# Kernel optimization log

Hardware: AMD Instinct MI355X
Metric: run time of the kernel (lower is better)

The kernel has to match this reference:

```python
import jax, jax.numpy as jnp
import numpy as np

EPS = 1e-6
NH, D_NOPE, D_ROPE, DV = 16, 128, 64, 128
DQK = D_NOPE + D_ROPE  # 192
KV_LORA = 512
Q_LORA = 1536
TOP_K, N_GROUP, TOPK_GROUP, N_EXP = 2, 4, 2, 8
INTER = 768
SCALING = DQK ** -0.5  # rope_scaling is None -> no yarn mscale
RSF = 2.5  # routed_scaling_factor


def rms_norm(x, w):
    v = jnp.mean(jnp.square(x), axis=-1, keepdims=True)
    return x * jax.lax.rsqrt(v + EPS) * w


def rotate_half(x):
    x1, x2 = jnp.split(x, 2, axis=-1)
    return jnp.concatenate([-x2, x1], axis=-1)


def interleave(x):
    # view(b,h,s,d//2,2).transpose(4,3).reshape(b,h,s,d): evens then odds
    b, h, s, d = x.shape
    return x.reshape(b, h, s, d // 2, 2).swapaxes(-1, -2).reshape(b, h, s, d)


def mlp(x, gw, uw, dw):
    return (jax.nn.silu(x @ gw.T) * (x @ uw.T)) @ dw.T


def setup_inputs() -> dict:
    key = jax.random.key(0)
    ks = jax.random.split(key, 16)
    B, S, H = 2, 1024, 2048
    sd = 0.02

    def p(k, shape):
        return jax.random.normal(k, shape, jnp.float32) * sd

    # standard RoPE cos/sin table
    inv_freq = 1.0 / (10000.0 ** (jnp.arange(0, D_ROPE, 2, dtype=jnp.float32) / D_ROPE))
    pos = jnp.arange(S, dtype=jnp.float32)
    freqs = pos[:, None] * inv_freq[None, :]
    emb = jnp.concatenate([freqs, freqs], axis=-1)  # [S, D_ROPE]
    cos = jnp.broadcast_to(jnp.cos(emb)[None], (B, S, D_ROPE))
    sin = jnp.broadcast_to(jnp.sin(emb)[None], (B, S, D_ROPE))

    return dict(
        hidden_states=jax.random.normal(ks[0], (B, S, H), jnp.float32),
        cos=cos,
        sin=sin,
        ln1_w=jnp.ones((H,), jnp.float32),
        q_a_w=p(ks[1], (Q_LORA, H)),
        q_a_ln_w=jnp.ones((Q_LORA,), jnp.float32),
        q_b_w=p(ks[2], (NH * DQK, Q_LORA)),
        kv_a_w=p(ks[3], (KV_LORA + D_ROPE, H)),
        kv_a_ln_w=jnp.ones((KV_LORA,), jnp.float32),
        kv_b_w=p(ks[4], (NH * (D_NOPE + DV), KV_LORA)),
        o_w=p(ks[5], (H, NH * DV)),
        ln2_w=jnp.ones((H,), jnp.float32),
        router_w=p(ks[6], (N_EXP, H)),
        router_bias=jnp.zeros((N_EXP,), jnp.float32),
        gate_w=p(ks[7], (N_EXP, INTER, H)),
        up_w=p(ks[8], (N_EXP, INTER, H)),
        down_w=p(ks[9], (N_EXP, H, INTER)),
        sh_gate_w=p(ks[10], (INTER, H)),
        sh_up_w=p(ks[11], (INTER, H)),
        sh_down_w=p(ks[12], (H, INTER)),
    )


def reference(hidden_states, cos, sin, ln1_w, q_a_w, q_a_ln_w, q_b_w, kv_a_w,
              kv_a_ln_w, kv_b_w, o_w, ln2_w, router_w, router_bias,
              gate_w, up_w, down_w, sh_gate_w, sh_up_w, sh_down_w):
    B, S, H = hidden_states.shape
    # ----- input_layernorm + MLA attention -----
    resid = hidden_states
    x = rms_norm(hidden_states, ln1_w)

    q = rms_norm(x @ q_a_w.T, q_a_ln_w) @ q_b_w.T       # [B,S,NH*DQK]
    q = q.reshape(B, S, NH, DQK).transpose(0, 2, 1, 3)   # [B,NH,S,DQK]
    q_pass, q_rot = q[..., :D_NOPE], q[..., D_NOPE:]

    ckv = x @ kv_a_w.T                                   # [B,S,KV_LORA+D_ROPE]
    k_pass_c, k_rot = ckv[..., :KV_LORA], ckv[..., KV_LORA:]
    kv = rms_norm(k_pass_c, kv_a_ln_w) @ kv_b_w.T        # [B,S,NH*(D_NOPE+DV)]
    kv = kv.reshape(B, S, NH, D_NOPE + DV).transpose(0, 2, 1, 3)
    k_pass, v = kv[..., :D_NOPE], kv[..., D_NOPE:]

    k_rot = k_rot.reshape(B, 1, S, D_ROPE)
    c = cos[:, None]  # [B,1,S,D_ROPE]
    s_ = sin[:, None]
    q_rot = interleave(q_rot)
    k_rot = interleave(k_rot)
    q_rot = q_rot * c + rotate_half(q_rot) * s_
    k_rot = k_rot * c + rotate_half(k_rot) * s_
    k_rot = jnp.broadcast_to(k_rot, (B, NH, S, D_ROPE))

    qs = jnp.concatenate([q_pass, q_rot], axis=-1)       # [B,NH,S,DQK]
    ks = jnp.concatenate([k_pass, k_rot], axis=-1)

    scores = jnp.einsum('bhqd,bhkd->bhqk', qs, ks) * SCALING
    causal = jnp.tril(jnp.ones((S, S), dtype=bool))
    scores = jnp.where(causal, scores, -jnp.inf)
    probs = jax.nn.softmax(scores, axis=-1)
    attn = jnp.einsum('bhqk,bhkd->bhqd', probs, v)
    attn = attn.transpose(0, 2, 1, 3).reshape(B, S, NH * DV)
    x = resid + attn @ o_w.T

    # ----- post_attention_layernorm + MoE -----
    resid = x
    h = rms_norm(x, ln2_w)
    t = h.reshape(-1, H)

    # router (fp32)
    scores_r = jax.nn.sigmoid(t.astype(jnp.float32) @ router_w.T.astype(jnp.float32))
    sc = scores_r + router_bias[None, :]
    gs = sc.reshape(-1, N_GROUP, N_EXP // N_GROUP)
    group_scores = jax.lax.top_k(gs, 2)[0].sum(-1)          # [T,G]
    gidx = jax.lax.top_k(group_scores, TOPK_GROUP)[1]
    gmask = jax.nn.one_hot(gidx, N_GROUP).sum(1)            # [T,G]
    emask = jnp.repeat(gmask, N_EXP // N_GROUP, axis=-1)    # [T,E]
    masked = jnp.where(emask > 0, sc, 0.0)
    idx = jax.lax.top_k(masked, TOP_K)[1]                   # [T,k]
    w = jnp.take_along_axis(scores_r, idx, axis=-1)
    w = w / (w.sum(-1, keepdims=True) + 1e-20) * RSF

    # routed experts: dense-all-experts compute, then routed-weight combine
    gate_h = jnp.einsum('td,eid->tei', t, gate_w)
    up_h = jnp.einsum('td,eid->tei', t, up_w)
    eo = jnp.einsum('tei,edi->ted', jax.nn.silu(gate_h) * up_h, down_w)
    dense_w = (jax.nn.one_hot(idx, N_EXP) * w[..., None]).sum(1)  # [T,E]
    moe_out = jnp.einsum('ted,te->td', eo, dense_w).reshape(B, S, H)

    shared = mlp(h, sh_gate_w, sh_up_w, sh_down_w)
    return resid + moe_out + shared
```

## Files before the change

### kernel.cpp

```cpp
#include <hip/hip_runtime.h>

typedef float f4 __attribute__((ext_vector_type(4)));
typedef float f32x4 __attribute__((ext_vector_type(4)));
typedef unsigned short us8 __attribute__((ext_vector_type(8)));
typedef __bf16 bf8 __attribute__((ext_vector_type(8)));

static constexpr int B_ = 2, S_ = 1024, H_ = 2048, T_ = B_ * S_;
static constexpr int NH_ = 16, DN_ = 128, DR_ = 64, DV_ = 128, DQK_ = 192;
static constexpr int KVL_ = 512, QL_ = 1536, INTER_ = 768, NEXP_ = 8, NE9_ = 9;
static constexpr int QKA_ = 2176;
static constexpr float SCALING_ = 0.07216878364870322f;
static constexpr float EPS_ = 1e-6f;

__device__ __forceinline__ unsigned short f2bf(float f) {
    unsigned u = __float_as_uint(f);
    u += 0x7fffu + ((u >> 16) & 1u);
    return (unsigned short)(u >> 16);
}
__device__ __forceinline__ float bf2f(unsigned short h) {
    return __uint_as_float(((unsigned)h) << 16);
}
__device__ __forceinline__ us8 pack8(f4 a, f4 b) {
    us8 r;
    r[0] = f2bf(a[0]); r[1] = f2bf(a[1]); r[2] = f2bf(a[2]); r[3] = f2bf(a[3]);
    r[4] = f2bf(b[0]); r[5] = f2bf(b[1]); r[6] = f2bf(b[2]); r[7] = f2bf(b[3]);
    return r;
}

__device__ __forceinline__ void gload16(const unsigned short* g, unsigned short* lds) {
    __builtin_amdgcn_global_load_lds(
        (const __attribute__((address_space(1))) void*)g,
        (__attribute__((address_space(3))) void*)lds, 16, 0, 0);
}

template <int MODE>
__global__ __launch_bounds__(256) void gemm2(
    const unsigned short* __restrict__ A, const unsigned short* __restrict__ Bw,
    float* __restrict__ Cf, unsigned short* __restrict__ Cb,
    const float* __restrict__ add,
    const int* __restrict__ cnt, const int* __restrict__ off,
    int M, int N, int K, int ldA, long sB)
{
    constexpr int BM = 128, BN = 128, BK = 64;
    __shared__ __align__(16) unsigned short As[2][BM * BK];
    __shared__ __align__(16) unsigned short Bs[2][BN * BK];
    const int tid = threadIdx.x, lane = tid & 63, wv = tid >> 6;
    const int wm = (wv >> 1) * 64, wn = (wv & 1) * 64;

    const int nb = gridDim.x * gridDim.y;
    const int lin = blockIdx.y * gridDim.x + blockIdx.x;
    const int swz = (lin & 7) * (nb >> 3) + (lin >> 3);
    const int bx = swz % gridDim.x;
    const int by = swz / gridDim.x;
    const int m0 = bx * BM, n0 = by * BN;

    int mcnt = M, obase = 0;
    if constexpr (MODE == 2) {
        mcnt = cnt[blockIdx.z];
        if (m0 >= mcnt) return;
        obase = off[blockIdx.z];
    }

    const int srow = tid >> 3;
    const int scol = (((tid & 7) ^ (srow & 7)) * 8);
    long aoff[4], boff[4];
#pragma unroll
    for (int s = 0; s < 4; s++) {
        int r = m0 + s * 32 + srow;
        if constexpr (MODE == 2) {
            aoff[s] = (long)(obase + r) * ldA + scol;
        } else {
            aoff[s] = (long)r * ldA + scol;
        }
        boff[s] = (long)blockIdx.z * sB + (long)(n0 + s * 32 + srow) * K + scol;
    }

    f32x4 acc[4][4];
#pragma unroll
    for (int m = 0; m < 4; m++)
#pragma unroll
        for (int n = 0; n < 4; n++) acc[m][n] = f32x4{0.f, 0.f, 0.f, 0.f};

    const int fr = lane & 15, lg = lane >> 4;
    const int xr = fr & 7;

    auto stage = [&](int buf, int k0) {
#pragma unroll
        for (int s = 0; s < 4; s++)
            gload16(A + aoff[s] + k0, &As[buf][s * 2048 + wv * 512]);
#pragma unroll
        for (int s = 0; s < 4; s++)
            gload16(Bw + boff[s] + k0, &Bs[buf][s * 2048 + wv * 512]);
    };
    auto compute = [&](int buf) {
        __builtin_amdgcn_s_setprio(1);
        bf8 af[4][2], bfv[4][2];
#pragma unroll
        for (int m = 0; m < 4; m++) {
            int R = wm + m * 16 + fr;
#pragma unroll
            for (int ks = 0; ks < 2; ks++)
                af[m][ks] = *(const bf8*)&As[buf][R * 64 + ((ks * 4 + lg) ^ xr) * 8];
        }
#pragma unroll
        for (int n = 0; n < 4; n++) {
            int R = wn + n * 16 + fr;
#pragma unroll
            for (int ks = 0; ks < 2; ks++)
                bfv[n][ks] = *(const bf8*)&Bs[buf][R * 64 + ((ks * 4 + lg) ^ xr) * 8];
        }
#pragma unroll
        for (int m = 0; m < 4; m++)
#pragma unroll
            for (int n = 0; n < 4; n++) {
                acc[m][n] = __builtin_amdgcn_mfma_f32_16x16x32_bf16(af[m][0], bfv[n][0], acc[m][n], 0, 0, 0);
                acc[m][n] = __builtin_amdgcn_mfma_f32_16x16x32_bf16(af[m][1], bfv[n][1], acc[m][n], 0, 0, 0);
            }
        __builtin_amdgcn_s_setprio(0);
    };

    const int nt = K / BK;
    stage(0, 0);
    for (int t = 0; t < nt; t++) {
        if (t + 1 < nt) {
            stage((t & 1) ^ 1, (t + 1) * BK);
            asm volatile("s_waitcnt vmcnt(8)" ::: "memory");
        } else {
            asm volatile("s_waitcnt vmcnt(0)" ::: "memory");
        }
        __builtin_amdgcn_s_barrier();
        compute(t & 1);
        __builtin_amdgcn_s_barrier();
    }

#pragma unroll
    for (int m = 0; m < 4; m++) {
#pragma unroll
        for (int n = 0; n < 4; n++) {
#pragma unroll
            for (int i = 0; i < 4; i++) {
                int row = wm + m * 16 + lg * 4 + i;
                int col = n0 + wn + n * 16 + fr;
                float v = acc[m][n][i];
                if constexpr (MODE == 0) {
                    long idx = (long)(m0 + row) * N + col;
                    if (Cb)       Cb[idx] = f2bf(v);
                    else if (add) Cf[idx] = v + add[idx];
                    else          Cf[idx] = v;
                } else {
                    if (m0 + row < mcnt)
                        Cb[(long)(obase + m0 + row) * N + col] = f2bf(v);
                }
            }
        }
    }
}

__global__ __launch_bounds__(256) void gemm_gu(
    const unsigned short* __restrict__ A, const unsigned short* __restrict__ Bw,
    unsigned short* __restrict__ actm,
    const int* __restrict__ cnt, const int* __restrict__ off,
    const int* __restrict__ idxl)
{
    constexpr int BM = 64, BN = 64, BK = 64, K = H_;
    __shared__ __align__(16) unsigned short As[2][BM * BK];
    __shared__ __align__(16) unsigned short Bg[2][BN * BK];
    __shared__ __align__(16) unsigned short Bu[2][BN * BK];
    const int tid = threadIdx.x, lane = tid & 63, wv = tid >> 6;
    const int wm = (wv >> 1) * 32, wn = (wv & 1) * 32;

    const int nb = gridDim.x * gridDim.y;
    const int lin = blockIdx.y * gridDim.x + blockIdx.x;
    const int swz = (lin & 7) * (nb >> 3) + (lin >> 3);
    const int bx = swz % gridDim.x;
    const int by = swz / gridDim.x;
    const int m0 = bx * BM, n0 = by * BN;
    const int e = blockIdx.z;

    const int mcnt = cnt[e];
    if (m0 >= mcnt) return;
    const int obase = off[e];

    const int srow = tid >> 3;
    const int scol = (((tid & 7) ^ (srow & 7)) * 8);
    long aoff[2], bgo[2], buo[2];
#pragma unroll
    for (int s = 0; s < 2; s++) {
        int r = m0 + s * 32 + srow;
        int rc = (r < mcnt) ? r : mcnt - 1;
        aoff[s] = (long)idxl[(long)e * T_ + rc] * H_ + scol;
        bgo[s] = ((long)e * (2 * INTER_) + n0 + s * 32 + srow) * K + scol;
        buo[s] = ((long)e * (2 * INTER_) + INTER_ + n0 + s * 32 + srow) * K + scol;
    }

    f32x4 ag[2][2], au[2][2];
#pragma unroll
    for (int m = 0; m < 2; m++)
#pragma unroll
        for (int n = 0; n < 2; n++) {
            ag[m][n] = f32x4{0.f, 0.f, 0.f, 0.f};
            au[m][n] = f32x4{0.f, 0.f, 0.f, 0.f};
        }

    const int fr = lane & 15, lg = lane >> 4;
    const int xr = fr & 7;

    auto stage = [&](int buf, int k0) {
#pragma unroll
        for (int s = 0; s < 2; s++)
            gload16(A + aoff[s] + k0, &As[buf][s * 2048 + wv * 512]);
#pragma unroll
        for (int s = 0; s < 2; s++)
            gload16(Bw + bgo[s] + k0, &Bg[buf][s * 2048 + wv * 512]);
#pragma unroll
        for (int s = 0; s < 2; s++)
            gload16(Bw + buo[s] + k0, &Bu[buf][s * 2048 + wv * 512]);
    };
    auto compute = [&](int buf) {
        __builtin_amdgcn_s_setprio(1);
        bf8 af[2][2], bgf[2][2], buf_[2][2];
#pragma unroll
        for (int m = 0; m < 2; m++) {
            int R = wm + m * 16 + fr;
#pragma unroll
            for (int ks = 0; ks < 2; ks++)
                af[m][ks] = *(const bf8*)&As[buf][R * 64 + ((ks * 4 + lg) ^ xr) * 8];
        }
#pragma unroll
        for (int n = 0; n < 2; n++) {
            int R = wn + n * 16 + fr;
#pragma unroll
            for (int ks = 0; ks < 2; ks++) {
                bgf[n][ks] = *(const bf8*)&Bg[buf][R * 64 + ((ks * 4 + lg) ^ xr) * 8];
                buf_[n][ks] = *(const bf8*)&Bu[buf][R * 64 + ((ks * 4 + lg) ^ xr) * 8];
            }
        }
#pragma unroll
        for (int m = 0; m < 2; m++)
#pragma unroll
            for (int n = 0; n < 2; n++) {
                ag[m][n] = __builtin_amdgcn_mfma_f32_16x16x32_bf16(af[m][0], bgf[n][0], ag[m][n], 0, 0, 0);
                ag[m][n] = __builtin_amdgcn_mfma_f32_16x16x32_bf16(af[m][1], bgf[n][1], ag[m][n], 0, 0, 0);
                au[m][n] = __builtin_amdgcn_mfma_f32_16x16x32_bf16(af[m][0], buf_[n][0], au[m][n], 0, 0, 0);
                au[m][n] = __builtin_amdgcn_mfma_f32_16x16x32_bf16(af[m][1], buf_[n][1], au[m][n], 0, 0, 0);
            }
        __builtin_amdgcn_s_setprio(0);
    };

    const int nt = K / BK;
    stage(0, 0);
    for (int t = 0; t < nt; t++) {
        if (t + 1 < nt) {
            stage((t & 1) ^ 1, (t + 1) * BK);
            asm volatile("s_waitcnt vmcnt(6)" ::: "memory");
        } else {
            asm volatile("s_waitcnt vmcnt(0)" ::: "memory");
        }
        __builtin_amdgcn_s_barrier();
        compute(t & 1);
        __builtin_amdgcn_s_barrier();
    }

#pragma unroll
    for (int m = 0; m < 2; m++) {
#pragma unroll
        for (int n = 0; n < 2; n++) {
#pragma unroll
            for (int i = 0; i < 4; i++) {
                int row = wm + m * 16 + lg * 4 + i;
                if (m0 + row < mcnt) {
                    float g = ag[m][n][i], u = au[m][n][i];
                    float v = g / (1.f + __expf(-g)) * u;
                    actm[(long)(obase + m0 + row) * INTER_ + n0 + wn + n * 16 + fr] = f2bf(v);
                }
            }
        }
    }
}

__global__ __launch_bounds__(256) void fa_k(
    const unsigned short* __restrict__ qs, const unsigned short* __restrict__ ks,
    const unsigned short* __restrict__ vt, unsigned short* __restrict__ ab)
{
    constexpr int KB = 64;
    const int q0 = blockIdx.x * 64;
    const int bh = blockIdx.y;
    const int b = bh >> 4, h = bh & 15;
    const int tid = threadIdx.x, lane = tid & 63, wv = tid >> 6;
    const int fr = lane & 15, lg = lane >> 4;
    const int ko = lg * 8;

    __shared__ __align__(16) unsigned short Kl[KB][200];
    __shared__ __align__(16) unsigned short Vl[128][72];
    __shared__ __align__(16) unsigned short Pl[4][16][72];

    const unsigned short* qp = qs + ((long)bh * S_ + q0 + wv * 16 + fr) * DQK_ + ko;
    bf8 qf[6];
#pragma unroll
    for (int s = 0; s < 6; s++) qf[s] = *(const bf8*)(qp + s * 32);

    f32x4 o[8];
#pragma unroll
    for (int n = 0; n < 8; n++) o[n] = f32x4{0.f, 0.f, 0.f, 0.f};
    float mrow[4] = {-3e38f, -3e38f, -3e38f, -3e38f};
    float lrow[4] = {0.f, 0.f, 0.f, 0.f};

    const int nt = q0 / KB + 1;

    const unsigned short* kg = ks + ((long)bh * S_ + (tid >> 2)) * DQK_ + (tid & 3) * 48;
    const unsigned short* vg = vt + ((long)bh * DV_ + (tid >> 1)) * S_ + (tid & 1) * 32;

    us8 krg[6], vrg[4];
#pragma unroll
    for (int j = 0; j < 6; j++) krg[j] = *(const us8*)(kg + j * 8);
#pragma unroll
    for (int j = 0; j < 4; j++) vrg[j] = *(const us8*)(vg + j * 8);

    for (int t = 0; t < nt; t++) {
        __syncthreads();
        {
            int r = tid >> 2, c = (tid & 3) * 48;
#pragma unroll
            for (int j = 0; j < 6; j++) *(us8*)&Kl[r][c + j * 8] = krg[j];
            int dv = tid >> 1, c2 = (tid & 1) * 32;
#pragma unroll
            for (int j = 0; j < 4; j++) *(us8*)&Vl[dv][c2 + j * 8] = vrg[j];
        }
        __syncthreads();
        if (t + 1 < nt) {
            long kof = (long)(t + 1) * KB;
#pragma unroll
            for (int j = 0; j < 6; j++) krg[j] = *(const us8*)(kg + kof * DQK_ + j * 8);
#pragma unroll
            for (int j = 0; j < 4; j++) vrg[j] = *(const us8*)(vg + kof + j * 8);
        }
        f32x4 ps[4];
#pragma unroll
        for (int ct = 0; ct < 4; ct++) {
            f32x4 a = f32x4{0.f, 0.f, 0.f, 0.f};
#pragma unroll
            for (int s = 0; s < 6; s++) {
                bf8 kf = *(const bf8*)&Kl[ct * 16 + fr][s * 32 + ko];
                a = __builtin_amdgcn_mfma_f32_16x16x32_bf16(qf[s], kf, a, 0, 0, 0);
            }
            ps[ct] = a;
        }
        const int kv0 = t * KB;
        const bool diag = (kv0 == q0);
#pragma unroll
        for (int ct = 0; ct < 4; ct++)
#pragma unroll
            for (int i = 0; i < 4; i++) {
                float v = ps[ct][i] * SCALING_;
                if (diag && (kv0 + ct * 16 + fr) > (q0 + wv * 16 + lg * 4 + i)) v = -3e38f;
                ps[ct][i] = v;
            }
        float scl[4];
#pragma unroll
        for (int i = 0; i < 4; i++) {
            float v = fmaxf(fmaxf(ps[0][i], ps[1][i]), fmaxf(ps[2][i], ps[3][i]));
#pragma unroll
            for (int x = 8; x; x >>= 1) v = fmaxf(v, __shfl_xor(v, x, 16));
            float mn = fmaxf(mrow[i], v);
            scl[i] = __expf(mrow[i] - mn);
            mrow[i] = mn;
        }
        float tsum[4] = {0.f, 0.f, 0.f, 0.f};
#pragma unroll
        for (int ct = 0; ct < 4; ct++)
#pragma unroll
            for (int i = 0; i < 4; i++) {
                float e = __expf(ps[ct][i] - mrow[i]);
                tsum[i] += e;
                Pl[wv][lg * 4 + i][ct * 16 + fr] = f2bf(e);
            }
#pragma unroll
        for (int i = 0; i < 4; i++) {
            float v = tsum[i];
#pragma unroll
            for (int x = 8; x; x >>= 1) v += __shfl_xor(v, x, 16);
            lrow[i] = lrow[i] * scl[i] + v;
        }
#pragma unroll
        for (int n = 0; n < 8; n++)
#pragma unroll
            for (int i = 0; i < 4; i++) o[n][i] *= scl[i];
        bf8 pf[2];
#pragma unroll
        for (int ksl = 0; ksl < 2; ksl++)
            pf[ksl] = *(const bf8*)&Pl[wv][fr][ksl * 32 + ko];
#pragma unroll
        for (int n = 0; n < 8; n++)
#pragma unroll
            for (int ksl = 0; ksl < 2; ksl++) {
                bf8 vf = *(const bf8*)&Vl[n * 16 + fr][ksl * 32 + ko];
                o[n] = __builtin_amdgcn_mfma_f32_16x16x32_bf16(pf[ksl], vf, o[n], 0, 0, 0);
            }
    }
#pragma unroll
    for (int i = 0; i < 4; i++) {
        float inv = 1.f / lrow[i];
        long rbase = ((long)b * S_ + q0 + wv * 16 + lg * 4 + i) * H_ + h * DV_;
#pragma unroll
        for (int n = 0; n < 8; n++)
            ab[rbase + n * 16 + fr] = f2bf(o[n][i] * inv);
    }
}

__global__ __launch_bounds__(256) void cvt_k(
    const float* __restrict__ s, unsigned short* __restrict__ d, long n)
{
    long i = ((long)blockIdx.x * 256 + threadIdx.x) * 8;
    if (i < n) {
        f4 a = *(const f4*)(s + i);
        f4 b = *(const f4*)(s + i + 4);
        *(us8*)(d + i) = pack8(a, b);
    }
}

__global__ __launch_bounds__(256) void cvt_qka_k(
    const float* __restrict__ qa, const float* __restrict__ kva,
    unsigned short* __restrict__ d)
{
    long i = ((long)blockIdx.x * 256 + threadIdx.x) * 8;
    long row = i >> 11, col = i & 2047;
    us8 o;
    if (row < QL_) {
        const float* s = qa + row * H_ + col;
        o = pack8(*(const f4*)s, *(const f4*)(s + 4));
    } else if (row < QL_ + 576) {
        const float* s = kva + (row - QL_) * H_ + col;
        o = pack8(*(const f4*)s, *(const f4*)(s + 4));
    } else {
        o = us8{0, 0, 0, 0, 0, 0, 0, 0};
    }
    *(us8*)(d + i) = o;
}

__global__ __launch_bounds__(256) void cvt_cat9_k(
    const float* __restrict__ g, const float* __restrict__ u,
    const float* __restrict__ sg, const float* __restrict__ su,
    unsigned short* __restrict__ d)
{
    long ii = ((long)blockIdx.x * 256 + threadIdx.x) * 8;
    int e = blockIdx.y;
    long row = ii >> 11, col = ii & 2047;
    const float* src;
    if (row < INTER_)
        src = (e < 8) ? (g + ((long)e * INTER_ + row) * H_ + col) : (sg + row * H_ + col);
    else
        src = (e < 8) ? (u + ((long)e * INTER_ + row - INTER_) * H_ + col)
                      : (su + (row - INTER_) * H_ + col);
    *(us8*)(d + (long)e * (2 * INTER_) * H_ + ii) = pack8(*(const f4*)src, *(const f4*)(src + 4));
}

__global__ __launch_bounds__(256) void rmsnorm_f2b(
    const float* __restrict__ in, const float* __restrict__ w,
    unsigned short* __restrict__ ob, float* __restrict__ of)
{
    const long base = (long)blockIdx.x * H_;
    const int c = threadIdx.x * 8;
    f4 v0 = *(const f4*)(in + base + c);
    f4 v1 = *(const f4*)(in + base + c + 4);
    float ss = v0[0] * v0[0] + v0[1] * v0[1] + v0[2] * v0[2] + v0[3] * v0[3]
             + v1[0] * v1[0] + v1[1] * v1[1] + v1[2] * v1[2] + v1[3] * v1[3];
#pragma unroll
    for (int o = 32; o; o >>= 1) ss += __shfl_down(ss, o);
    __shared__ float red[4];
    if ((threadIdx.x & 63) == 0) red[threadIdx.x >> 6] = ss;
    __syncthreads();
    float r = rsqrtf((red[0] + red[1] + red[2] + red[3]) / H_ + EPS_);
    f4 w0 = *(const f4*)(w + c);
    f4 w1 = *(const f4*)(w + c + 4);
    f4 a, b;
#pragma unroll
    for (int j = 0; j < 4; j++) { a[j] = v0[j] * r * w0[j]; b[j] = v1[j] * r * w1[j]; }
    *(us8*)(ob + base + c) = pack8(a, b);
    if (of) {
        *(f4*)(of + base + c) = a;
        *(f4*)(of + base + c + 4) = b;
    }
}

__global__ __launch_bounds__(256) void rmsnorm_b2b(
    const unsigned short* __restrict__ in, const float* __restrict__ w,
    unsigned short* __restrict__ out, int cols, int istride, int ostride)
{
    const long ib = (long)blockIdx.x * istride;
    const long ob = (long)blockIdx.x * ostride;
    const int nu = cols >> 3;
    float ss = 0.f;
    for (int u = threadIdx.x; u < nu; u += 256) {
        us8 v = *(const us8*)(in + ib + u * 8);
#pragma unroll
        for (int j = 0; j < 8; j++) { float f = bf2f(v[j]); ss += f * f; }
    }
#pragma unroll
    for (int o = 32; o; o >>= 1) ss += __shfl_down(ss, o);
    __shared__ float red[4];
    if ((threadIdx.x & 63) == 0) red[threadIdx.x >> 6] = ss;
    __syncthreads();
    float r = rsqrtf((red[0] + red[1] + red[2] + red[3]) / cols + EPS_);
    for (int u = threadIdx.x; u < nu; u += 256) {
        us8 v = *(const us8*)(in + ib + u * 8);
        f4 w0 = *(const f4*)(w + u * 8);
        f4 w1 = *(const f4*)(w + u * 8 + 4);
        us8 o;
#pragma unroll
        for (int j = 0; j < 4; j++) o[j] = f2bf(bf2f(v[j]) * r * w0[j]);
#pragma unroll
        for (int j = 0; j < 4; j++) o[4 + j] = f2bf(bf2f(v[4 + j]) * r * w1[j]);
        *(us8*)(out + ob + u * 8) = o;
    }
}

__global__ __launch_bounds__(64) void rope_q_k(
    const unsigned short* __restrict__ q, const float* __restrict__ cs,
    const float* __restrict__ sn, unsigned short* __restrict__ qs)
{
    int t = blockIdx.x;
    int h = t & 15;
    int bs = t >> 4;
    int s = bs & (S_ - 1);
    int b = bs >> 10;
    const unsigned short* qrow = q + (long)bs * (NH_ * DQK_) + h * DQK_;
    unsigned short* orow = qs + ((long)(b * NH_ + h) * S_ + s) * DQK_;
    int l = threadIdx.x;
    orow[l] = qrow[l];
    orow[l + 64] = qrow[l + 64];
    int j = l & 31;
    float x0 = bf2f(qrow[DN_ + 2 * j]), x1 = bf2f(qrow[DN_ + 2 * j + 1]);
    float c = cs[(long)bs * DR_ + j], si = sn[(long)bs * DR_ + j];
    if (l < 32) orow[DN_ + j] = f2bf(x0 * c - x1 * si);
    else        orow[DN_ + 32 + j] = f2bf(x1 * c + x0 * si);
}

__global__ __launch_bounds__(64) void rope_k_k(
    const unsigned short* __restrict__ qkab, const float* __restrict__ cs,
    const float* __restrict__ sn, unsigned short* __restrict__ ks)
{
    int bs = blockIdx.x;
    int s = bs & (S_ - 1);
    int b = bs >> 10;
    const unsigned short* kr = qkab + (long)bs * QKA_ + QL_ + KVL_;
    int l = threadIdx.x;
    int j = l & 31;
    float x0 = bf2f(kr[2 * j]), x1 = bf2f(kr[2 * j + 1]);
    float c = cs[(long)bs * DR_ + j], si = sn[(long)bs * DR_ + j];
    float val = (l < 32) ? (x0 * c - x1 * si) : (x1 * c + x0 * si);
    int off = (l < 32) ? (DN_ + j) : (DN_ + 32 + j);
    unsigned short bv = f2bf(val);
    for (int h = 0; h < NH_; h++)
        ks[((long)(b * NH_ + h) * S_ + s) * DQK_ + off] = bv;
}

__global__ __launch_bounds__(128) void kpass_k(
    const unsigned short* __restrict__ kv, unsigned short* __restrict__ ks)
{
    int t = blockIdx.x;
    int h = t & 15;
    int bs = t >> 4;
    int s = bs & (S_ - 1);
    int b = bs >> 10;
    ks[((long)(b * NH_ + h) * S_ + s) * DQK_ + threadIdx.x] = kv[(long)t * 256 + threadIdx.x];
}

__global__ __launch_bounds__(256) void vt_k(
    const unsigned short* __restrict__ kv, unsigned short* __restrict__ vt)
{
    __shared__ unsigned short tile[64][DV_ + 8];
    int s0 = blockIdx.x * 64;
    int bh = blockIdx.y;
    int b = bh >> 4, h = bh & 15;
#pragma unroll
    for (int it = 0; it < 4; it++) {
        int idx = it * 256 + threadIdx.x;
        int sl = idx >> 4, du = idx & 15;
        *(us8*)&tile[sl][du * 8] =
            *(const us8*)(kv + ((long)(b * S_ + s0 + sl) * NH_ + h) * 256 + DN_ + du * 8);
    }
    __syncthreads();
#pragma unroll
    for (int it = 0; it < 4; it++) {
        int idx = it * 256 + threadIdx.x;
        int d = idx >> 3, su = idx & 7;
        us8 o;
#pragma unroll
        for (int j = 0; j < 8; j++) o[j] = tile[su * 8 + j][d];
        *(us8*)(vt + ((long)bh * DV_ + d) * S_ + s0 + su * 8) = o;
    }
}

__global__ void zero9_k(int* __restrict__ cnt)
{
    if (threadIdx.x < NE9_) cnt[threadIdx.x] = (threadIdx.x == 8) ? T_ : 0;
}

__global__ void offs_k(const int* __restrict__ cnt, int* __restrict__ off)
{
    if (threadIdx.x == 0) {
        int a = 0;
        for (int e = 0; e < NE9_; e++) { off[e] = a; a += cnt[e]; }
    }
}

__global__ __launch_bounds__(64) void router_k(
    const float* __restrict__ h, const float* __restrict__ rw,
    const float* __restrict__ rb, int* __restrict__ cnt,
    int* __restrict__ idxl, int* __restrict__ tep, float* __restrict__ tww)
{
    int t = blockIdx.x;
    int l = threadIdx.x;
    const float* hr = h + (long)t * H_;
    float pe[8] = {0, 0, 0, 0, 0, 0, 0, 0};
    for (int k = l; k < H_; k += 64) {
        float hv = hr[k];
#pragma unroll
        for (int e = 0; e < 8; e++) pe[e] += hv * rw[e * H_ + k];
    }
#pragma unroll
    for (int e = 0; e < 8; e++)
        for (int o = 32; o; o >>= 1) pe[e] += __shfl_down(pe[e], o);
    if (l == 0) {
        float sr[8], sc[8];
#pragma unroll
        for (int e = 0; e < 8; e++) {
            sr[e] = 1.f / (1.f + __expf(-pe[e]));
            sc[e] = sr[e] + rb[e];
        }
        float gs[4];
        for (int g = 0; g < 4; g++) gs[g] = sc[2 * g] + sc[2 * g + 1];
        int g0 = 0;
        for (int g = 1; g < 4; g++) if (gs[g] > gs[g0]) g0 = g;
        int g1 = -1;
        for (int g = 0; g < 4; g++) {
            if (g == g0) continue;
            if (g1 < 0 || gs[g] > gs[g1]) g1 = g;
        }
        int i0 = -1, i1 = -1;
        for (int e = 0; e < 8; e++) {
            int g = e >> 1;
            if (g != g0 && g != g1) continue;
            if (i0 < 0 || sc[e] > sc[i0]) i0 = e;
        }
        for (int e = 0; e < 8; e++) {
            int g = e >> 1;
            if (g != g0 && g != g1) continue;
            if (e == i0) continue;
            if (i1 < 0 || sc[e] > sc[i1]) i1 = e;
        }
        float w0 = sr[i0], w1 = sr[i1];
        float inv = 2.5f / (w0 + w1 + 1e-20f);
        int p0 = atomicAdd(&cnt[i0], 1);
        idxl[i0 * T_ + p0] = t;
        int p1 = atomicAdd(&cnt[i1], 1);
        idxl[i1 * T_ + p1] = t;
        tep[t * 4 + 0] = i0; tep[t * 4 + 1] = p0;
        tep[t * 4 + 2] = i1; tep[t * 4 + 3] = p1;
        tww[t * 2 + 0] = w0 * inv;
        tww[t * 2 + 1] = w1 * inv;
        idxl[8 * T_ + t] = t;
    }
}

__global__ __launch_bounds__(256) void gather_k(
    const unsigned short* __restrict__ pd, const int* __restrict__ off,
    const int* __restrict__ tep, const float* __restrict__ tww,
    float* __restrict__ out)
{
    int t = blockIdx.x;
    int e0 = tep[t * 4], p0 = tep[t * 4 + 1];
    int e1 = tep[t * 4 + 2], p1 = tep[t * 4 + 3];
    float w0 = tww[t * 2], w1 = tww[t * 2 + 1];
    long r0 = (long)(off[e0] + p0) * H_;
    long r1 = (long)(off[e1] + p1) * H_;
    long rs = (long)(off[8] + t) * H_;
    int c = threadIdx.x * 8;
    us8 a = *(const us8*)(pd + r0 + c);
    us8 b = *(const us8*)(pd + r1 + c);
    us8 s = *(const us8*)(pd + rs + c);
    float* op = out + (long)t * H_ + c;
#pragma unroll
    for (int j = 0; j < 8; j++)
        op[j] += bf2f(s[j]) + w0 * bf2f(a[j]) + w1 * bf2f(b[j]);
}

extern "C" void kernel_launch(void* const* d_in, const int* in_sizes, int n_in,
                              void* d_out, int out_size, void* d_ws, size_t ws_size,
                              hipStream_t stream)
{
    const float* hidden = (const float*)d_in[0];
    const float* cosb   = (const float*)d_in[1];
    const float* sinb   = (const float*)d_in[2];
    const float* ln1w   = (const float*)d_in[3];
    const float* qaw    = (const float*)d_in[4];
    const float* qalnw  = (const float*)d_in[5];
    const float* qbw    = (const float*)d_in[6];
    const float* kvaw   = (const float*)d_in[7];
    const float* kvalnw = (const float*)d_in[8];
    const float* kvbw   = (const float*)d_in[9];
    const float* ow     = (const float*)d_in[10];
    const float* ln2w   = (const float*)d_in[11];
    const float* rw     = (const float*)d_in[12];
    const float* rb     = (const float*)d_in[13];
    const float* gw     = (const float*)d_in[14];
    const float* uw     = (const float*)d_in[15];
    const float* dwn    = (const float*)d_in[16];
    const float* sgw    = (const float*)d_in[17];
    const float* suw    = (const float*)d_in[18];
    const float* sdw    = (const float*)d_in[19];
    float* out = (float*)d_out;
    (void)in_sizes; (void)n_in; (void)out_size; (void)ws_size;

    char* ws = (char*)d_ws;
    const size_t MB = 1u << 20;
    unsigned short* qkawb = (unsigned short*)(ws + 0 * MB);
    unsigned short* qbwb  = (unsigned short*)(ws + 9 * MB);
    unsigned short* kvbwb = (unsigned short*)(ws + 18 * MB);
    unsigned short* owb   = (unsigned short*)(ws + 22 * MB);
    unsigned short* xb    = (unsigned short*)(ws + 30 * MB);
    unsigned short* qkab  = (unsigned short*)(ws + 38 * MB);
    unsigned short* qb16  = (unsigned short*)(ws + 47 * MB);
    unsigned short* ckvnb = (unsigned short*)(ws + 59 * MB);
    unsigned short* kvb   = (unsigned short*)(ws + 61 * MB);
    unsigned short* qs    = (unsigned short*)(ws + 77 * MB);
    unsigned short* ks    = (unsigned short*)(ws + 89 * MB);
    unsigned short* vt    = (unsigned short*)(ws + 30 * MB);
    unsigned short* ab    = (unsigned short*)(ws + 38 * MB);
    float* hbuf = (float*)(ws + 0 * MB);
    unsigned short* actm = (unsigned short*)(ws + 0 * MB);
    unsigned short* hb16 = (unsigned short*)(ws + 16 * MB);
    int*   cnt  = (int*)(ws + 24 * MB);
    int*   offb = (int*)(ws + 24 * MB + 256);
    int*   idxl = (int*)(ws + 24 * MB + 512);
    int*   tep  = (int*)(ws + 24 * MB + 512 + 9 * T_ * 4);
    float* tww  = (float*)(ws + 24 * MB + 512 + 9 * T_ * 4 + 4 * T_ * 4);
    unsigned short* guwb = (unsigned short*)(ws + 25 * MB);
    unsigned short* dwnb = (unsigned short*)(ws + 25 * MB);
    unsigned short* pd   = (unsigned short*)(ws + 79 * MB);

    cvt_qka_k<<<(QKA_ * H_) / 2048, 256, 0, stream>>>(qaw, kvaw, qkawb);
    cvt_k<<<(NH_ * DQK_ * QL_) / 2048, 256, 0, stream>>>(qbw, qbwb, (long)NH_ * DQK_ * QL_);
    cvt_k<<<(NH_ * 256 * KVL_) / 2048, 256, 0, stream>>>(kvbw, kvbwb, (long)NH_ * 256 * KVL_);
    cvt_k<<<(H_ * H_) / 2048, 256, 0, stream>>>(ow, owb, (long)H_ * H_);

    rmsnorm_f2b<<<T_, 256, 0, stream>>>(hidden, ln1w, xb, nullptr);

    gemm2<0><<<dim3(T_ / 128, QKA_ / 128, 1), 256, 0, stream>>>(
        xb, qkawb, nullptr, qkab, nullptr, nullptr, nullptr,
        T_, QKA_, H_, H_, 0);
    rmsnorm_b2b<<<T_, 256, 0, stream>>>(qkab, qalnw, qkab, QL_, QKA_, QKA_);
    gemm2<0><<<dim3(T_ / 128, (NH_ * DQK_) / 128, 1), 256, 0, stream>>>(
        qkab, qbwb, nullptr, qb16, nullptr, nullptr, nullptr,
        T_, NH_ * DQK_, QL_, QKA_, 0);
    rmsnorm_b2b<<<T_, 256, 0, stream>>>(qkab + QL_, kvalnw, ckvnb, KVL_, QKA_, KVL_);
    gemm2<0><<<dim3(T_ / 128, (NH_ * 256) / 128, 1), 256, 0, stream>>>(
        ckvnb, kvbwb, nullptr, kvb, nullptr, nullptr, nullptr,
        T_, NH_ * 256, KVL_, KVL_, 0);

    rope_q_k<<<T_ * NH_, 64, 0, stream>>>(qb16, cosb, sinb, qs);
    rope_k_k<<<T_, 64, 0, stream>>>(qkab, cosb, sinb, ks);
    kpass_k<<<T_ * NH_, 128, 0, stream>>>(kvb, ks);
    vt_k<<<dim3(S_ / 64, B_ * NH_), 256, 0, stream>>>(kvb, vt);

    fa_k<<<dim3(S_ / 64, B_ * NH_), 256, 0, stream>>>(qs, ks, vt, ab);

    gemm2<0><<<dim3(T_ / 128, H_ / 128, 1), 256, 0, stream>>>(
        ab, owb, out, nullptr, hidden, nullptr, nullptr,
        T_, H_, H_, H_, 0);

    rmsnorm_f2b<<<T_, 256, 0, stream>>>(out, ln2w, hb16, hbuf);
    zero9_k<<<1, 64, 0, stream>>>(cnt);
    router_k<<<T_, 64, 0, stream>>>(hbuf, rw, rb, cnt, idxl, tep, tww);
    offs_k<<<1, 64, 0, stream>>>(cnt, offb);

    cvt_cat9_k<<<dim3((2 * INTER_ * H_) / 2048, NE9_), 256, 0, stream>>>(gw, uw, sgw, suw, guwb);
    gemm_gu<<<dim3(T_ / 64, INTER_ / 64, NE9_), 256, 0, stream>>>(
        hb16, guwb, actm, cnt, offb, idxl);

    cvt_k<<<(NEXP_ * H_ * INTER_) / 2048, 256, 0, stream>>>(dwn, dwnb, (long)NEXP_ * H_ * INTER_);
    cvt_k<<<(H_ * INTER_) / 2048, 256, 0, stream>>>(sdw, dwnb + (long)NEXP_ * H_ * INTER_, (long)H_ * INTER_);

    gemm2<2><<<dim3(T_ / 128, H_ / 128, NE9_), 256, 0, stream>>>(
        actm, dwnb, nullptr, pd, nullptr, cnt, offb,
        T_, H_, INTER_, INTER_, (long)H_ * INTER_);
    gather_k<<<T_, 256, 0, stream>>>(pd, offb, tep, tww, out);
}
```

Measured before the change: 501.0 us.

## Fuse fp32 weight conversion into GEMM B-tile loads and reverse FA block order

Drops the separate fp32-to-bf16 weight conversion kernels for q_b, kv_b, o_proj, the expert gate/up and the down weights. The GEMMs now load fp32 weights into registers, pack them to bf16 and write them to LDS inside the double-buffered loop. This removes a full read-write pass over the weights and several launches. The cost is twice the B-tile global traffic per reuse, more registers, and a direct LDS write path instead of global_load_lds. The attention grid also reverses the query-block order for half the heads, presumably to balance causal workload across CUs.

```diff
diff --git a/kernel.cpp b/kernel.cpp
--- a/kernel.cpp
+++ b/kernel.cpp
@@ -33,9 +33,10 @@
         (__attribute__((address_space(3))) void*)lds, 16, 0, 0);
 }
 
-template <int MODE>
+template <int MODE, int BF32>
 __global__ __launch_bounds__(256) void gemm2(
-    const unsigned short* __restrict__ A, const unsigned short* __restrict__ Bw,
+    const unsigned short* __restrict__ A, const void* __restrict__ Bv,
+    const void* __restrict__ Bv2,
     float* __restrict__ Cf, unsigned short* __restrict__ Cb,
     const float* __restrict__ add,
     const int* __restrict__ cnt, const int* __restrict__ off,
@@ -61,6 +62,16 @@
         obase = off[blockIdx.z];
     }
 
+    const unsigned short* Bb = (const unsigned short*)Bv;
+    const float* Bf = nullptr;
+    if constexpr (BF32) {
+        if constexpr (MODE == 2)
+            Bf = (blockIdx.z < 8) ? ((const float*)Bv + (long)blockIdx.z * sB)
+                                  : (const float*)Bv2;
+        else
+            Bf = (const float*)Bv;
+    }
+
     const int srow = tid >> 3;
     const int scol = (((tid & 7) ^ (srow & 7)) * 8);
     long aoff[4], boff[4];
@@ -72,7 +83,10 @@
         } else {
             aoff[s] = (long)r * ldA + scol;
         }
-        boff[s] = (long)blockIdx.z * sB + (long)(n0 + s * 32 + srow) * K + scol;
+        if constexpr (BF32)
+            boff[s] = (long)(n0 + s * 32 + srow) * K + scol;
+        else
+            boff[s] = (long)blockIdx.z * sB + (long)(n0 + s * 32 + srow) * K + scol;
     }
 
     f32x4 acc[4][4];
@@ -84,13 +98,23 @@
     const int fr = lane & 15, lg = lane >> 4;
     const int xr = fr & 7;
 
-    auto stage = [&](int buf, int k0) {
+    auto stageA = [&](int buf, int k0) {
 #pragma unroll
         for (int s = 0; s < 4; s++)
             gload16(A + aoff[s] + k0, &As[buf][s * 2048 + wv * 512]);
+    };
+    f4 brg[4][2];
+    auto issueB = [&](int k0) {
+#pragma unroll
+        for (int s = 0; s < 4; s++) {
+            brg[s][0] = *(const f4*)(Bf + boff[s] + k0);
+            brg[s][1] = *(const f4*)(Bf + boff[s] + k0 + 4);
+        }
+    };
+    auto writeB = [&](int buf) {
 #pragma unroll
         for (int s = 0; s < 4; s++)
-            gload16(Bw + boff[s] + k0, &Bs[buf][s * 2048 + wv * 512]);
+            *(us8*)&Bs[buf][s * 2048 + srow * 64 + (tid & 7) * 8] = pack8(brg[s][0], brg[s][1]);
     };
     auto compute = [&](int buf) {
         __builtin_amdgcn_s_setprio(1);
@@ -120,17 +144,45 @@
     };
 
     const int nt = K / BK;
-    stage(0, 0);
-    for (int t = 0; t < nt; t++) {
-        if (t + 1 < nt) {
-            stage((t & 1) ^ 1, (t + 1) * BK);
-            asm volatile("s_waitcnt vmcnt(8)" ::: "memory");
-        } else {
-            asm volatile("s_waitcnt vmcnt(0)" ::: "memory");
-        }
-        __builtin_amdgcn_s_barrier();
-        compute(t & 1);
-        __builtin_amdgcn_s_barrier();
+    if constexpr (BF32 == 0) {
+        auto stageB = [&](int buf, int k0) {
+#pragma unroll
+            for (int s = 0; s < 4; s++)
+                gload16(Bb + boff[s] + k0, &Bs[buf][s * 2048 + wv * 512]);
+        };
+        stageA(0, 0);
+        stageB(0, 0);
+        for (int t = 0; t < nt; t++) {
+            if (t + 1 < nt) {
+                stageA((t & 1) ^ 1, (t + 1) * BK);
+                stageB((t & 1) ^ 1, (t + 1) * BK);
+                asm volatile("s_waitcnt vmcnt(8)" ::: "memory");
+            } else {
+                asm volatile("s_waitcnt vmcnt(0)" ::: "memory");
+            }
+            __builtin_amdgcn_s_barrier();
+            compute(t & 1);
+            __builtin_amdgcn_s_barrier();
+        }
+    } else {
+        issueB(0);
+        stageA(0, 0);
+        writeB(0);
+        asm volatile("s_waitcnt lgkmcnt(0)" ::: "memory");
+        for (int t = 0; t < nt; t++) {
+            if (t + 1 < nt) {
+                issueB((t + 1) * BK);
+                stageA((t & 1) ^ 1, (t + 1) * BK);
+                asm volatile("s_waitcnt vmcnt(12)" ::: "memory");
+            } else {
+                asm volatile("s_waitcnt vmcnt(0)" ::: "memory");
+            }
+            __builtin_amdgcn_s_barrier();
+            compute(t & 1);
+            if (t + 1 < nt) writeB((t & 1) ^ 1);
+            asm volatile("s_waitcnt lgkmcnt(0)" ::: "memory");
+            __builtin_amdgcn_s_barrier();
+        }
     }
 
 #pragma unroll
@@ -157,7 +209,9 @@
 }
 
 __global__ __launch_bounds__(256) void gemm_gu(
-    const unsigned short* __restrict__ A, const unsigned short* __restrict__ Bw,
+    const unsigned short* __restrict__ A,
+    const float* __restrict__ gw, const float* __restrict__ uw,
+    const float* __restrict__ sgw, const float* __restrict__ suw,
     unsigned short* __restrict__ actm,
     const int* __restrict__ cnt, const int* __restrict__ off,
     const int* __restrict__ idxl)
@@ -181,16 +235,18 @@
     if (m0 >= mcnt) return;
     const int obase = off[e];
 
+    const float* gW = (e < 8) ? (gw + (long)e * INTER_ * H_) : sgw;
+    const float* uW = (e < 8) ? (uw + (long)e * INTER_ * H_) : suw;
+
     const int srow = tid >> 3;
     const int scol = (((tid & 7) ^ (srow & 7)) * 8);
-    long aoff[2], bgo[2], buo[2];
+    long aoff[2], bro[2];
 #pragma unroll
     for (int s = 0; s < 2; s++) {
         int r = m0 + s * 32 + srow;
         int rc = (r < mcnt) ? r : mcnt - 1;
         aoff[s] = (long)idxl[(long)e * T_ + rc] * H_ + scol;
-        bgo[s] = ((long)e * (2 * INTER_) + n0 + s * 32 + srow) * K + scol;
-        buo[s] = ((long)e * (2 * INTER_) + INTER_ + n0 + s * 32 + srow) * K + scol;
+        bro[s] = (long)(n0 + s * 32 + srow) * K + scol;
     }
 
     f32x4 ag[2][2], au[2][2];
@@ -205,16 +261,27 @@
     const int fr = lane & 15, lg = lane >> 4;
     const int xr = fr & 7;
 
-    auto stage = [&](int buf, int k0) {
+    auto stageA = [&](int buf, int k0) {
 #pragma unroll
         for (int s = 0; s < 2; s++)
             gload16(A + aoff[s] + k0, &As[buf][s * 2048 + wv * 512]);
-#pragma unroll
-        for (int s = 0; s < 2; s++)
-            gload16(Bw + bgo[s] + k0, &Bg[buf][s * 2048 + wv * 512]);
-#pragma unroll
-        for (int s = 0; s < 2; s++)
-            gload16(Bw + buo[s] + k0, &Bu[buf][s * 2048 + wv * 512]);
+    };
+    f4 brg[4][2];
+    auto issueB = [&](int k0) {
+#pragma unroll
+        for (int s = 0; s < 2; s++) {
+            brg[s][0] = *(const f4*)(gW + bro[s] + k0);
+            brg[s][1] = *(const f4*)(gW + bro[s] + k0 + 4);
+            brg[2 + s][0] = *(const f4*)(uW + bro[s] + k0);
+            brg[2 + s][1] = *(const f4*)(uW + bro[s] + k0 + 4);
+        }
+    };
+    auto writeB = [&](int buf) {
+#pragma unroll
+        for (int s = 0; s < 2; s++) {
+            *(us8*)&Bg[buf][s * 2048 + (srow & 31) * 64 + (tid & 7) * 8] = pack8(brg[s][0], brg[s][1]);
+            *(us8*)&Bu[buf][s * 2048 + (srow & 31) * 64 + (tid & 7) * 8] = pack8(brg[2 + s][0], brg[2 + s][1]);
+        }
     };
     auto compute = [&](int buf) {
         __builtin_amdgcn_s_setprio(1);
@@ -248,16 +315,22 @@
     };
 
     const int nt = K / BK;
-    stage(0, 0);
+    issueB(0);
+    stageA(0, 0);
+    writeB(0);
+    asm volatile("s_waitcnt lgkmcnt(0)" ::: "memory");
     for (int t = 0; t < nt; t++) {
         if (t + 1 < nt) {
-            stage((t & 1) ^ 1, (t + 1) * BK);
-            asm volatile("s_waitcnt vmcnt(6)" ::: "memory");
+            issueB((t + 1) * BK);
+            stageA((t & 1) ^ 1, (t + 1) * BK);
+            asm volatile("s_waitcnt vmcnt(10)" ::: "memory");
         } else {
             asm volatile("s_waitcnt vmcnt(0)" ::: "memory");
         }
         __builtin_amdgcn_s_barrier();
         compute(t & 1);
+        if (t + 1 < nt) writeB((t & 1) ^ 1);
+        asm volatile("s_waitcnt lgkmcnt(0)" ::: "memory");
         __builtin_amdgcn_s_barrier();
     }
 
@@ -283,7 +356,8 @@
     const unsigned short* __restrict__ vt, unsigned short* __restrict__ ab)
 {
     constexpr int KB = 64;
-    const int q0 = blockIdx.x * 64;
+    const int qx = (blockIdx.y & 16) ? (gridDim.x - 1 - (int)blockIdx.x) : (int)blockIdx.x;
+    const int q0 = qx * 64;
     const int bh = blockIdx.y;
     const int b = bh >> 4, h = bh & 15;
     const int tid = threadIdx.x, lane = tid & 63, wv = tid >> 6;
@@ -404,17 +478,6 @@
 #pragma unroll
         for (int n = 0; n < 8; n++)
             ab[rbase + n * 16 + fr] = f2bf(o[n][i] * inv);
-    }
-}
-
-__global__ __launch_bounds__(256) void cvt_k(
-    const float* __restrict__ s, unsigned short* __restrict__ d, long n)
-{
-    long i = ((long)blockIdx.x * 256 + threadIdx.x) * 8;
-    if (i < n) {
-        f4 a = *(const f4*)(s + i);
-        f4 b = *(const f4*)(s + i + 4);
-        *(us8*)(d + i) = pack8(a, b);
     }
 }
 
@@ -435,23 +498,6 @@
         o = us8{0, 0, 0, 0, 0, 0, 0, 0};
     }
     *(us8*)(d + i) = o;
-}
-
-__global__ __launch_bounds__(256) void cvt_cat9_k(
-    const float* __restrict__ g, const float* __restrict__ u,
-    const float* __restrict__ sg, const float* __restrict__ su,
-    unsigned short* __restrict__ d)
-{
-    long ii = ((long)blockIdx.x * 256 + threadIdx.x) * 8;
-    int e = blockIdx.y;
-    long row = ii >> 11, col = ii & 2047;
-    const float* src;
-    if (row < INTER_)
-        src = (e < 8) ? (g + ((long)e * INTER_ + row) * H_ + col) : (sg + row * H_ + col);
-    else
-        src = (e < 8) ? (u + ((long)e * INTER_ + row - INTER_) * H_ + col)
-                      : (su + (row - INTER_) * H_ + col);
-    *(us8*)(d + (long)e * (2 * INTER_) * H_ + ii) = pack8(*(const f4*)src, *(const f4*)(src + 4));
 }
 
 __global__ __launch_bounds__(256) void rmsnorm_f2b(
@@ -715,9 +761,6 @@
     char* ws = (char*)d_ws;
     const size_t MB = 1u << 20;
     unsigned short* qkawb = (unsigned short*)(ws + 0 * MB);
-    unsigned short* qbwb  = (unsigned short*)(ws + 9 * MB);
-    unsigned short* kvbwb = (unsigned short*)(ws + 18 * MB);
-    unsigned short* owb   = (unsigned short*)(ws + 22 * MB);
     unsigned short* xb    = (unsigned short*)(ws + 30 * MB);
     unsigned short* qkab  = (unsigned short*)(ws + 38 * MB);
     unsigned short* qb16  = (unsigned short*)(ws + 47 * MB);
@@ -735,27 +778,22 @@
     int*   idxl = (int*)(ws + 24 * MB + 512);
     int*   tep  = (int*)(ws + 24 * MB + 512 + 9 * T_ * 4);
     float* tww  = (float*)(ws + 24 * MB + 512 + 9 * T_ * 4 + 4 * T_ * 4);
-    unsigned short* guwb = (unsigned short*)(ws + 25 * MB);
-    unsigned short* dwnb = (unsigned short*)(ws + 25 * MB);
-    unsigned short* pd   = (unsigned short*)(ws + 79 * MB);
+    unsigned short* pd   = (unsigned short*)(ws + 25 * MB);
 
     cvt_qka_k<<<(QKA_ * H_) / 2048, 256, 0, stream>>>(qaw, kvaw, qkawb);
-    cvt_k<<<(NH_ * DQK_ * QL_) / 2048, 256, 0, stream>>>(qbw, qbwb, (long)NH_ * DQK_ * QL_);
-    cvt_k<<<(NH_ * 256 * KVL_) / 2048, 256, 0, stream>>>(kvbw, kvbwb, (long)NH_ * 256 * KVL_);
-    cvt_k<<<(H_ * H_) / 2048, 256, 0, stream>>>(ow, owb, (long)H_ * H_);
 
     rmsnorm_f2b<<<T_, 256, 0, stream>>>(hidden, ln1w, xb, nullptr);
 
-    gemm2<0><<<dim3(T_ / 128, QKA_ / 128, 1), 256, 0, stream>>>(
-        xb, qkawb, nullptr, qkab, nullptr, nullptr, nullptr,
+    gemm2<0, 0><<<dim3(T_ / 128, QKA_ / 128, 1), 256, 0, stream>>>(
+        xb, qkawb, nullptr, nullptr, qkab, nullptr, nullptr, nullptr,
         T_, QKA_, H_, H_, 0);
     rmsnorm_b2b<<<T_, 256, 0, stream>>>(qkab, qalnw, qkab, QL_, QKA_, QKA_);
-    gemm2<0><<<dim3(T_ / 128, (NH_ * DQK_) / 128, 1), 256, 0, stream>>>(
-        qkab, qbwb, nullptr, qb16, nullptr, nullptr, nullptr,
+    gemm2<0, 1><<<dim3(T_ / 128, (NH_ * DQK_) / 128, 1), 256, 0, stream>>>(
+        qkab, qbw, nullptr, nullptr, qb16, nullptr, nullptr, nullptr,
         T_, NH_ * DQK_, QL_, QKA_, 0);
     rmsnorm_b2b<<<T_, 256, 0, stream>>>(qkab + QL_, kvalnw, ckvnb, KVL_, QKA_, KVL_);
-    gemm2<0><<<dim3(T_ / 128, (NH_ * 256) / 128, 1), 256, 0, stream>>>(
-        ckvnb, kvbwb, nullptr, kvb, nullptr, nullptr, nullptr,
+    gemm2<0, 1><<<dim3(T_ / 128, (NH_ * 256) / 128, 1), 256, 0, stream>>>(
+        ckvnb, kvbw, nullptr, nullptr, kvb, nullptr, nullptr, nullptr,
         T_, NH_ * 256, KVL_, KVL_, 0);
 
     rope_q_k<<<T_ * NH_, 64, 0, stream>>>(qb16, cosb, sinb, qs);
@@ -765,8 +803,8 @@
 
     fa_k<<<dim3(S_ / 64, B_ * NH_), 256, 0, stream>>>(qs, ks, vt, ab);
 
-    gemm2<0><<<dim3(T_ / 128, H_ / 128, 1), 256, 0, stream>>>(
-        ab, owb, out, nullptr, hidden, nullptr, nullptr,
+    gemm2<0, 1><<<dim3(T_ / 128, H_ / 128, 1), 256, 0, stream>>>(
+        ab, ow, nullptr, out, nullptr, hidden, nullptr, nullptr,
         T_, H_, H_, H_, 0);
 
     rmsnorm_f2b<<<T_, 256, 0, stream>>>(out, ln2w, hb16, hbuf);
@@ -774,15 +812,11 @@
     router_k<<<T_, 64, 0, stream>>>(hbuf, rw, rb, cnt, idxl, tep, tww);
     offs_k<<<1, 64, 0, stream>>>(cnt, offb);
 
-    cvt_cat9_k<<<dim3((2 * INTER_ * H_) / 2048, NE9_), 256, 0, stream>>>(gw, uw, sgw, suw, guwb);
     gemm_gu<<<dim3(T_ / 64, INTER_ / 64, NE9_), 256, 0, stream>>>(
-        hb16, guwb, actm, cnt, offb, idxl);
-
-    cvt_k<<<(NEXP_ * H_ * INTER_) / 2048, 256, 0, stream>>>(dwn, dwnb, (long)NEXP_ * H_ * INTER_);
-    cvt_k<<<(H_ * INTER_) / 2048, 256, 0, stream>>>(sdw, dwnb + (long)NEXP_ * H_ * INTER_, (long)H_ * INTER_);
-
-    gemm2<2><<<dim3(T_ / 128, H_ / 128, NE9_), 256, 0, stream>>>(
-        actm, dwnb, nullptr, pd, nullptr, cnt, offb,
+        hb16, gw, uw, sgw, suw, actm, cnt, offb, idxl);
+
+    gemm2<2, 1><<<dim3(T_ / 128, H_ / 128, NE9_), 256, 0, stream>>>(
+        actm, dwn, sdw, nullptr, pd, nullptr, cnt, offb,
         T_, H_, INTER_, INTER_, (long)H_ * INTER_);
     gather_k<<<T_, 256, 0, stream>>>(pd, offb, tep, tww, out);
 }
```

After: 541.4 us. +8.1%, slower.
